# Optimization experiments

Measured on AMD Instinct MI355X. Metric: run time of the kernel, lower is better.

## Reference

```python
import jax, jax.numpy as jnp
import numpy as np

B, N, C, H = 4, 1024, 1024, 16
D = C // H  # head_dim = 64


def _xavier(key, shape, gain):
    fan_in, fan_out = shape[1], shape[0]
    limit = gain * np.sqrt(6.0 / (fan_in + fan_out))
    return jax.random.uniform(key, shape, jnp.float32, -limit, limit)


def setup_inputs() -> dict:
    key = jax.random.key(0)
    ks = jax.random.split(key, 12)
    g = 2.0 ** (-0.5)
    return {
        "x": jax.random.normal(ks[0], (B, N, C), jnp.float32),
        "attn_bias": jax.random.normal(ks[1], (B, H, N, N), jnp.float32),
        "attn_mask": jnp.ones((B, N), jnp.int32),
        "Wq": _xavier(ks[2], (C, C), g), "bq": jnp.zeros((C,), jnp.float32),
        "Wk": _xavier(ks[3], (C, C), g), "bk": jnp.zeros((C,), jnp.float32),
        "Wv": _xavier(ks[4], (C, C), g), "bv": jnp.zeros((C,), jnp.float32),
        "Wo": _xavier(ks[5], (C, C), 1.0), "bo": jnp.zeros((C,), jnp.float32),
    }


def reference(x, attn_bias, attn_mask, Wq, bq, Wk, bk, Wv, bv, Wo, bo):
    scale = D ** (-0.5)
    # projections; nn.Linear computes x @ W.T + b
    def proj(W, b):
        return (x @ W.T + b).reshape(B, N, H, D).transpose(0, 2, 1, 3)  # [B,H,N,D]
    q = proj(Wq, bq) * scale
    k = proj(Wk, bk)
    v = proj(Wv, bv)
    scores = jnp.einsum("bhnd,bhmd->bhnm", q, k)  # [B,H,N,N]
    scores = scores + attn_bias  # attn_bias_type == 'add'
    # 2D mask [B,N] -> [B,1,1,N]; masked_fill where mask == 0
    mask = attn_mask[:, None, None, :]
    scores = jnp.where(mask == 0, -jnp.inf, scores)
    weights = jax.nn.softmax(scores, axis=-1)  # stable (internal max subtract)
    # attn_drop is identity in eval / p=0.0
    out = jnp.einsum("bhnm,bhmd->bhnd", weights, v)
    out = out.transpose(0, 2, 1, 3).reshape(B, N, C)
    return out @ Wo.T + bo
```

## Files before the change

### kernel.cpp

```cpp
#include <hip/hip_runtime.h>
#include <hip/hip_bf16.h>

#define B_ 4
#define N_ 1024
#define C_ 1024
#define H_ 16
#define D_ 64

typedef __attribute__((ext_vector_type(8))) short bf16x8;
typedef __attribute__((ext_vector_type(4))) float f32x4;
typedef __attribute__((ext_vector_type(4))) int i32x4;

__device__ __forceinline__ void gld_lds16(const void* g, void* l) {
    __builtin_amdgcn_global_load_lds(
        (const __attribute__((address_space(1))) void*)g,
        (__attribute__((address_space(3))) void*)l, 16, 0, 0);
}

__device__ __forceinline__ unsigned cvt_pk_bf16(float lo, float hi) {
    unsigned r;
    asm("v_cvt_pk_bf16_f32 %0, %1, %2" : "=v"(r) : "v"(lo), "v"(hi));
    return r;
}

__global__ __launch_bounds__(256) void f2b_kernel(const float* __restrict__ s,
                                                  __hip_bfloat16* __restrict__ d,
                                                  int n) {
    int i = (blockIdx.x * 256 + threadIdx.x) * 4;
    if (i < n) {
        float4 v = *(const float4*)&s[i];
        d[i + 0] = __float2bfloat16(v.x);
        d[i + 1] = __float2bfloat16(v.y);
        d[i + 2] = __float2bfloat16(v.z);
        d[i + 3] = __float2bfloat16(v.w);
    }
}

__global__ __launch_bounds__(256) void f2b4_kernel(const float* __restrict__ w0,
                                                   const float* __restrict__ w1,
                                                   const float* __restrict__ w2,
                                                   const float* __restrict__ w3,
                                                   __hip_bfloat16* __restrict__ d0,
                                                   __hip_bfloat16* __restrict__ d1,
                                                   __hip_bfloat16* __restrict__ d2,
                                                   __hip_bfloat16* __restrict__ d3) {
    int sel = blockIdx.y;
    const float* s = sel == 0 ? w0 : sel == 1 ? w1 : sel == 2 ? w2 : w3;
    __hip_bfloat16* d = sel == 0 ? d0 : sel == 1 ? d1 : sel == 2 ? d2 : d3;
    int i = (blockIdx.x * 256 + threadIdx.x) * 4;
    float4 v = *(const float4*)&s[i];
    d[i + 0] = __float2bfloat16(v.x);
    d[i + 1] = __float2bfloat16(v.y);
    d[i + 2] = __float2bfloat16(v.z);
    d[i + 3] = __float2bfloat16(v.w);
}

__global__ __launch_bounds__(256) void gemm_qkv(const __hip_bfloat16* __restrict__ A,
                                                const __hip_bfloat16* __restrict__ wq,
                                                const __hip_bfloat16* __restrict__ wk,
                                                const __hip_bfloat16* __restrict__ wv,
                                                const float* __restrict__ bq,
                                                const float* __restrict__ bk,
                                                const float* __restrict__ bv,
                                                __hip_bfloat16* __restrict__ qo,
                                                __hip_bfloat16* __restrict__ ko,
                                                __hip_bfloat16* __restrict__ vto) {
    __shared__ __hip_bfloat16 Al[128 * 32];
    __shared__ __hip_bfloat16 Bl[128 * 32];
    const int sel = blockIdx.x >> 3;
    const __hip_bfloat16* Bw = sel == 0 ? wq : sel == 1 ? wk : wv;
    const float* bias = sel == 0 ? bq : sel == 1 ? bk : bv;
    const int t = threadIdx.x, w = t >> 6, l = t & 63;
    const int wr = w >> 1, wc = w & 1, lr = l & 15, lg = l >> 4;
    const int m0 = blockIdx.y * 128, n0 = (blockIdx.x & 7) * 128;
    const int K = C_;

    f32x4 acc[4][4] = {};

    for (int k0 = 0; k0 < K; k0 += 32) {
#pragma unroll
        for (int it = 0; it < 2; ++it) {
            int i = t + it * 256;
            int r = i >> 2, c8 = (i & 3) * 8;
            gld_lds16(A + (size_t)(m0 + r) * K + k0 + c8, &Al[i * 8]);
            gld_lds16(Bw + (size_t)(n0 + r) * K + k0 + c8, &Bl[i * 8]);
        }
        __syncthreads();
        bf16x8 af[4], bfr[4];
#pragma unroll
        for (int mi = 0; mi < 4; ++mi)
            af[mi] = *(const bf16x8*)&Al[(wr * 64 + mi * 16 + lr) * 32 + lg * 8];
#pragma unroll
        for (int ni = 0; ni < 4; ++ni)
            bfr[ni] = *(const bf16x8*)&Bl[(wc * 64 + ni * 16 + lr) * 32 + lg * 8];
#pragma unroll
        for (int mi = 0; mi < 4; ++mi)
#pragma unroll
            for (int ni = 0; ni < 4; ++ni)
                acc[mi][ni] = __builtin_amdgcn_mfma_f32_16x16x32_bf16(
                    af[mi], bfr[ni], acc[mi][ni], 0, 0, 0);
        __syncthreads();
    }

#pragma unroll
    for (int mi = 0; mi < 4; ++mi) {
#pragma unroll
        for (int ni = 0; ni < 4; ++ni) {
            int col = n0 + wc * 64 + ni * 16 + lr;
            float bb = bias[col];
#pragma unroll
            for (int j = 0; j < 4; ++j) {
                int row = m0 + wr * 64 + mi * 16 + lg * 4 + j;
                float v = acc[mi][ni][j] + bb;
                int bb_ = row >> 10, nn = row & 1023;
                int hh = col >> 6, dd = col & 63;
                if (sel == 0) {
                    qo[(((size_t)bb_ * H_ + hh) * N_ + nn) * D_ + dd] =
                        __float2bfloat16(v * 0.125f);
                } else if (sel == 1) {
                    ko[(((size_t)bb_ * H_ + hh) * N_ + nn) * D_ + dd] =
                        __float2bfloat16(v);
                } else {
                    vto[(((size_t)bb_ * H_ + hh) * D_ + dd) * N_ + nn] =
                        __float2bfloat16(v);
                }
            }
        }
    }
}

__global__ __launch_bounds__(256) void gemm_out(const __hip_bfloat16* __restrict__ A,
                                                const __hip_bfloat16* __restrict__ Bw,
                                                const float* __restrict__ bias,
                                                float* __restrict__ out) {
    __shared__ __hip_bfloat16 Al[128 * 32];
    __shared__ __hip_bfloat16 Bl[128 * 32];
    const int t = threadIdx.x, w = t >> 6, l = t & 63;
    const int wr = w >> 1, wc = w & 1, lr = l & 15, lg = l >> 4;
    const int m0 = blockIdx.y * 128, n0 = blockIdx.x * 128;
    const int K = C_;

    f32x4 acc[4][4] = {};

    for (int k0 = 0; k0 < K; k0 += 32) {
#pragma unroll
        for (int it = 0; it < 2; ++it) {
            int i = t + it * 256;
            int r = i >> 2, c8 = (i & 3) * 8;
            gld_lds16(A + (size_t)(m0 + r) * K + k0 + c8, &Al[i * 8]);
            gld_lds16(Bw + (size_t)(n0 + r) * K + k0 + c8, &Bl[i * 8]);
        }
        __syncthreads();
        bf16x8 af[4], bfr[4];
#pragma unroll
        for (int mi = 0; mi < 4; ++mi)
            af[mi] = *(const bf16x8*)&Al[(wr * 64 + mi * 16 + lr) * 32 + lg * 8];
#pragma unroll
        for (int ni = 0; ni < 4; ++ni)
            bfr[ni] = *(const bf16x8*)&Bl[(wc * 64 + ni * 16 + lr) * 32 + lg * 8];
#pragma unroll
        for (int mi = 0; mi < 4; ++mi)
#pragma unroll
            for (int ni = 0; ni < 4; ++ni)
                acc[mi][ni] = __builtin_amdgcn_mfma_f32_16x16x32_bf16(
                    af[mi], bfr[ni], acc[mi][ni], 0, 0, 0);
        __syncthreads();
    }

#pragma unroll
    for (int mi = 0; mi < 4; ++mi)
#pragma unroll
        for (int ni = 0; ni < 4; ++ni) {
            int col = n0 + wc * 64 + ni * 16 + lr;
            float bb = bias[col];
#pragma unroll
            for (int j = 0; j < 4; ++j) {
                int row = m0 + wr * 64 + mi * 16 + lg * 4 + j;
                out[(size_t)row * C_ + col] = acc[mi][ni][j] + bb;
            }
        }
}

#define ATTN_ITER(KT, CB, SB)                                                      \
    {                                                                              \
        const int ktn_ = (KT) < 15 ? (KT) + 1 : 15;                                \
        gld_lds16(kg0 + (size_t)ktn_ * 4096, &Kl[SB][(w * 64) * 8]);               \
        gld_lds16(vg0 + ktn_ * 64, &Vl[SB][(w * 64) * 8]);                         \
        __builtin_amdgcn_sched_barrier(0);                                         \
        asm volatile("s_waitcnt vmcnt(6)" ::: "memory");                           \
        __builtin_amdgcn_sched_barrier(0);                                         \
        __builtin_amdgcn_s_barrier();                                              \
        __builtin_amdgcn_sched_barrier(0);                                         \
        const __hip_bfloat16* Kb = &Kl[CB][0];                                     \
        f32x4 a_[4];                                                               \
        __builtin_amdgcn_s_setprio(1);                                             \
        _Pragma("unroll")                                                          \
        for (int nkb = 0; nkb < 4; ++nkb) {                                        \
            f32x4 a = {};                                                          \
            _Pragma("unroll")                                                      \
            for (int half = 0; half < 2; ++half) {                                 \
                bf16x8 kf = *(const bf16x8*)                                       \
                    &Kb[(nkb * 16 + lr) * 64 + ((half * 32 + lg * 8) ^ swz)];      \
                a = __builtin_amdgcn_mfma_f32_16x16x32_bf16(kf, qf[half], a,       \
                                                            0, 0, 0);              \
            }                                                                      \
            a_[nkb] = a;                                                           \
        }                                                                          \
        __builtin_amdgcn_s_setprio(0);                                             \
        __builtin_amdgcn_sched_barrier(0);                                         \
        asm volatile("s_waitcnt vmcnt(2)" ::: "memory");                           \
        __builtin_amdgcn_sched_barrier(0);                                         \
        float s[4][4];                                                             \
        _Pragma("unroll")                                                          \
        for (int nkb = 0; nkb < 4; ++nkb) {                                        \
            f32x4 bb = *(const f32x4*)&Bb[w][lr][((nkb * 4 + lg) ^ lr) * 4];       \
            f32x4 pen = *(const f32x4*)&Pen[(KT) * 64 + nkb * 16 + lg * 4];        \
            _Pragma("unroll")                                                      \
            for (int j = 0; j < 4; ++j) s[nkb][j] = a_[nkb][j] + bb[j] + pen[j];   \
        }                                                                          \
        __builtin_amdgcn_sched_barrier(0);                                         \
        asm volatile("s_waitcnt lgkmcnt(0)" ::: "memory");                         \
        __builtin_amdgcn_sched_barrier(0);                                         \
        _Pragma("unroll")                                                          \
        for (int i_ = 0; i_ < 4; ++i_)                                             \
            gld_lds16(bg[i_] + ktn_ * 64, bl + i_ * 256);                          \
        __builtin_amdgcn_sched_barrier(0);                                         \
        float tm = s[0][0];                                                        \
        _Pragma("unroll")                                                          \
        for (int nkb = 0; nkb < 4; ++nkb)                                          \
            _Pragma("unroll")                                                      \
            for (int j = 0; j < 4; ++j) tm = fmaxf(tm, s[nkb][j]);                 \
        tm = fmaxf(tm, __shfl_xor(tm, 16));                                        \
        tm = fmaxf(tm, __shfl_xor(tm, 32));                                        \
        const float mn = fmaxf(m_, tm);                                            \
        const float al = __expf(m_ - mn);                                          \
        m_ = mn;                                                                   \
        float ts = 0.f;                                                            \
        _Pragma("unroll")                                                          \
        for (int nkb = 0; nkb < 4; ++nkb)                                          \
            _Pragma("unroll")                                                      \
            for (int j = 0; j < 4; ++j) {                                          \
                float p = __expf(s[nkb][j] - mn);                                  \
                s[nkb][j] = p;                                                     \
                ts += p;                                                           \
            }                                                                      \
        ts += __shfl_xor(ts, 16);                                                  \
        ts += __shfl_xor(ts, 32);                                                  \
        l_ = l_ * al + ts;                                                         \
        unsigned pk0[4], pk1[4];                                                   \
        _Pragma("unroll")                                                          \
        for (int nkb = 0; nkb < 4; ++nkb) {                                        \
            pk0[nkb] = cvt_pk_bf16(s[nkb][0], s[nkb][1]);                          \
            pk1[nkb] = cvt_pk_bf16(s[nkb][2], s[nkb][3]);                          \
        }                                                                          \
        float alr[4];                                                              \
        _Pragma("unroll")                                                          \
        for (int j = 0; j < 4; ++j) alr[j] = __shfl(al, lg * 4 + j);               \
        _Pragma("unroll")                                                          \
        for (int db = 0; db < 4; ++db)                                             \
            _Pragma("unroll")                                                      \
            for (int j = 0; j < 4; ++j) acc[db][j] *= alr[j];                      \
        const __hip_bfloat16* Vb = &Vl[CB][0];                                     \
        __builtin_amdgcn_s_setprio(1);                                             \
        _Pragma("unroll")                                                          \
        for (int mh = 0; mh < 2; ++mh) {                                           \
            const int n0_ = 2 * mh, n1_ = 2 * mh + 1;                              \
            int e0a = __shfl((int)pk0[n0_], shi0), e0b = __shfl((int)pk0[n1_], shi0); \
            int e1a = __shfl((int)pk1[n0_], shi0), e1b = __shfl((int)pk1[n1_], shi0); \
            int e2a = __shfl((int)pk0[n0_], shi1), e2b = __shfl((int)pk0[n1_], shi1); \
            int e3a = __shfl((int)pk1[n0_], shi1), e3b = __shfl((int)pk1[n1_], shi1); \
            i32x4 pw;                                                              \
            pw[0] = lghi ? e0b : e0a;                                              \
            pw[1] = lghi ? e1b : e1a;                                              \
            pw[2] = lghi ? e2b : e2a;                                              \
            pw[3] = lghi ? e3b : e3a;                                              \
            bf16x8 paf = *(bf16x8*)&pw;                                            \
            _Pragma("unroll")                                                      \
            for (int db = 0; db < 4; ++db) {                                       \
                bf16x8 vf = *(const bf16x8*)                                       \
                    &Vb[(db * 16 + lr) * 64 + ((mh * 32 + lg * 8) ^ swz)];         \
                acc[db] = __builtin_amdgcn_mfma_f32_16x16x32_bf16(paf, vf,         \
                                                                  acc[db], 0, 0,  \
                                                                  0);              \
            }                                                                      \
        }                                                                          \
        __builtin_amdgcn_s_setprio(0);                                             \
        __builtin_amdgcn_sched_barrier(0);                                         \
        __builtin_amdgcn_s_barrier();                                              \
        __builtin_amdgcn_sched_barrier(0);                                         \
    }

__global__ __launch_bounds__(512, 4) void attn_kernel(const __hip_bfloat16* __restrict__ q,
                                                      const __hip_bfloat16* __restrict__ k,
                                                      const __hip_bfloat16* __restrict__ vt,
                                                      const float* __restrict__ bias,
                                                      const int* __restrict__ mask,
                                                      __hip_bfloat16* __restrict__ ao) {
    const int orig = blockIdx.x;
    const int wg = (orig & 7) * 64 + (orig >> 3);
    const int qt = wg & 7, h = (wg >> 3) & 15, b = wg >> 7;
    const int t = threadIdx.x, w = t >> 6, l = t & 63;
    const int lr = l & 15, lg = l >> 4;

    __shared__ __hip_bfloat16 Kl[2][64 * 64];
    __shared__ __hip_bfloat16 Vl[2][64 * 64];
    __shared__ float Pen[1024];
    __shared__ float Bb[8][16][64];

    const size_t bh = (size_t)b * H_ + h;
    const int qr0 = qt * 128;
    const int myrow = qr0 + w * 16 + lr;
    const int orow_base = qr0 + w * 16 + lg * 4;

    {
        int2 mi = *(const int2*)&mask[b * N_ + t * 2];
        float2 p;
        p.x = mi.x ? 0.f : -1e30f;
        p.y = mi.y ? 0.f : -1e30f;
        *(float2*)&Pen[t * 2] = p;
    }
    __syncthreads();

    const int r0 = t >> 3;
    const int e0 = ((t & 7) * 8) ^ ((r0 & 7) << 3);
    const __hip_bfloat16* kg0 = k + (bh * N_ + r0) * D_ + e0;
    const __hip_bfloat16* vg0 = vt + (bh * D_ + r0) * N_ + e0;

    const int rb = l >> 4, pb = l & 15;
    const float* bg[4];
#pragma unroll
    for (int i = 0; i < 4; ++i) {
        int ri = i * 4 + rb;
        bg[i] = bias + ((size_t)bh * N_ + qr0 + w * 16 + ri) * N_ + (pb ^ ri) * 4;
    }
    float* bl = &Bb[w][0][0];

    bf16x8 qf[2];
#pragma unroll
    for (int half = 0; half < 2; ++half)
        qf[half] = *(const bf16x8*)&q[(bh * N_ + myrow) * D_ + half * 32 + lg * 8];

    const int swz = (lr & 7) << 3;
    const int shi0 = ((lg & 1) << 5) + lr;
    const int shi1 = shi0 + 16;
    const bool lghi = (lg >> 1) != 0;

    f32x4 acc[4] = {};
    float m_ = -3e38f, l_ = 0.f;

    __builtin_amdgcn_sched_barrier(0);
    gld_lds16(kg0, &Kl[0][(w * 64) * 8]);
    gld_lds16(vg0, &Vl[0][(w * 64) * 8]);
#pragma unroll
    for (int i = 0; i < 4; ++i) gld_lds16(bg[i], bl + i * 256);
    __builtin_amdgcn_sched_barrier(0);

    for (int kt = 0; kt < 16; kt += 2) {
        ATTN_ITER(kt, 0, 1);
        ATTN_ITER(kt + 1, 1, 0);
    }

    float linv[4];
#pragma unroll
    for (int j = 0; j < 4; ++j) linv[j] = 1.f / __shfl(l_, lg * 4 + j);
#pragma unroll
    for (int db = 0; db < 4; ++db)
#pragma unroll
        for (int j = 0; j < 4; ++j)
            ao[((size_t)b * N_ + orow_base + j) * C_ + h * 64 + db * 16 + lr] =
                __float2bfloat16(acc[db][j] * linv[j]);
}

extern "C" void kernel_launch(void* const* d_in, const int* in_sizes, int n_in,
                              void* d_out, int out_size, void* d_ws, size_t ws_size,
                              hipStream_t stream) {
    const float* x    = (const float*)d_in[0];
    const float* bias = (const float*)d_in[1];
    const int*   mask = (const int*)d_in[2];
    const float* Wq   = (const float*)d_in[3];
    const float* bq   = (const float*)d_in[4];
    const float* Wk   = (const float*)d_in[5];
    const float* bk   = (const float*)d_in[6];
    const float* Wv   = (const float*)d_in[7];
    const float* bv   = (const float*)d_in[8];
    const float* Wo   = (const float*)d_in[9];
    const float* bo   = (const float*)d_in[10];
    float* out = (float*)d_out;

    char* ws = (char*)d_ws;
    const size_t MB = 1u << 20;
    __hip_bfloat16* xb  = (__hip_bfloat16*)(ws + 0 * MB);
    __hip_bfloat16* wqb = (__hip_bfloat16*)(ws + 8 * MB);
    __hip_bfloat16* wkb = (__hip_bfloat16*)(ws + 10 * MB);
    __hip_bfloat16* wvb = (__hip_bfloat16*)(ws + 12 * MB);
    __hip_bfloat16* wob = (__hip_bfloat16*)(ws + 14 * MB);
    __hip_bfloat16* qb  = (__hip_bfloat16*)(ws + 16 * MB);
    __hip_bfloat16* kb  = (__hip_bfloat16*)(ws + 24 * MB);
    __hip_bfloat16* vtb = (__hip_bfloat16*)(ws + 32 * MB);
    __hip_bfloat16* aob = (__hip_bfloat16*)(ws + 40 * MB);

    f2b_kernel<<<4096, 256, 0, stream>>>(x, xb, B_ * N_ * C_);
    f2b4_kernel<<<dim3(1024, 4), 256, 0, stream>>>(Wq, Wk, Wv, Wo, wqb, wkb, wvb, wob);

    gemm_qkv<<<dim3(24, 32), 256, 0, stream>>>(xb, wqb, wkb, wvb, bq, bk, bv, qb, kb, vtb);

    attn_kernel<<<512, 512, 0, stream>>>(qb, kb, vtb, bias, mask, aob);

    gemm_out<<<dim3(8, 32), 256, 0, stream>>>(aob, wob, bo, out);
}
```

Measured before the change: 154.0 us.

## Prefetch attention bias into registers and triple-buffer K/V to drop a barrier

Attention bias tiles now go straight from global memory into a two-deep register double buffer, loaded two tiles ahead, instead of being staged through a per-wave LDS buffer with extra waitcnts. K/V LDS buffers go from two to three, so the trailing workgroup barrier at the end of each tile iteration can be removed, and the loop is unrolled by six. This cuts LDS traffic and synchronisation for the bias. The cost is more vector registers, less coalesced per-row bias reads, and reliance on compiler-inserted vmcnt waits next to the hand-placed vmcnt(6).

```diff
diff --git a/kernel.cpp b/kernel.cpp
--- a/kernel.cpp
+++ b/kernel.cpp
@@ -181,9 +181,10 @@
         }
 }
 
-#define ATTN_ITER(KT, CB, SB)                                                      \
+#define ATTN_ITER(KT, CB, SB, BCUR)                                                \
     {                                                                              \
         const int ktn_ = (KT) < 15 ? (KT) + 1 : 15;                                \
+        const int ktb_ = (KT) < 14 ? (KT) + 2 : 15;                                \
         gld_lds16(kg0 + (size_t)ktn_ * 4096, &Kl[SB][(w * 64) * 8]);               \
         gld_lds16(vg0 + ktn_ * 64, &Vl[SB][(w * 64) * 8]);                         \
         __builtin_amdgcn_sched_barrier(0);                                         \
@@ -192,7 +193,7 @@
         __builtin_amdgcn_s_barrier();                                              \
         __builtin_amdgcn_sched_barrier(0);                                         \
         const __hip_bfloat16* Kb = &Kl[CB][0];                                     \
-        f32x4 a_[4];                                                               \
+        float s[4][4];                                                             \
         __builtin_amdgcn_s_setprio(1);                                             \
         _Pragma("unroll")                                                          \
         for (int nkb = 0; nkb < 4; ++nkb) {                                        \
@@ -204,26 +205,15 @@
                 a = __builtin_amdgcn_mfma_f32_16x16x32_bf16(kf, qf[half], a,       \
                                                             0, 0, 0);              \
             }                                                                      \
-            a_[nkb] = a;                                                           \
+            f32x4 pen = *(const f32x4*)&Pen[(KT) * 64 + nkb * 16 + lg * 4];        \
+            _Pragma("unroll")                                                      \
+            for (int j = 0; j < 4; ++j) s[nkb][j] = a[j] + BCUR[nkb][j] + pen[j];  \
         }                                                                          \
         __builtin_amdgcn_s_setprio(0);                                             \
         __builtin_amdgcn_sched_barrier(0);                                         \
-        asm volatile("s_waitcnt vmcnt(2)" ::: "memory");                           \
-        __builtin_amdgcn_sched_barrier(0);                                         \
-        float s[4][4];                                                             \
-        _Pragma("unroll")                                                          \
-        for (int nkb = 0; nkb < 4; ++nkb) {                                        \
-            f32x4 bb = *(const f32x4*)&Bb[w][lr][((nkb * 4 + lg) ^ lr) * 4];       \
-            f32x4 pen = *(const f32x4*)&Pen[(KT) * 64 + nkb * 16 + lg * 4];        \
-            _Pragma("unroll")                                                      \
-            for (int j = 0; j < 4; ++j) s[nkb][j] = a_[nkb][j] + bb[j] + pen[j];   \
-        }                                                                          \
-        __builtin_amdgcn_sched_barrier(0);                                         \
-        asm volatile("s_waitcnt lgkmcnt(0)" ::: "memory");                         \
-        __builtin_amdgcn_sched_barrier(0);                                         \
-        _Pragma("unroll")                                                          \
-        for (int i_ = 0; i_ < 4; ++i_)                                             \
-            gld_lds16(bg[i_] + ktn_ * 64, bl + i_ * 256);                          \
+        _Pragma("unroll")                                                          \
+        for (int nkb = 0; nkb < 4; ++nkb)                                          \
+            BCUR[nkb] = *(const f32x4*)&brow[ktb_ * 64 + nkb * 16 + lg * 4];       \
         __builtin_amdgcn_sched_barrier(0);                                         \
         float tm = s[0][0];                                                        \
         _Pragma("unroll")                                                          \
@@ -286,8 +276,6 @@
         }                                                                          \
         __builtin_amdgcn_s_setprio(0);                                             \
         __builtin_amdgcn_sched_barrier(0);                                         \
-        __builtin_amdgcn_s_barrier();                                              \
-        __builtin_amdgcn_sched_barrier(0);                                         \
     }
 
 __global__ __launch_bounds__(512, 4) void attn_kernel(const __hip_bfloat16* __restrict__ q,
@@ -302,10 +290,9 @@
     const int t = threadIdx.x, w = t >> 6, l = t & 63;
     const int lr = l & 15, lg = l >> 4;
 
-    __shared__ __hip_bfloat16 Kl[2][64 * 64];
-    __shared__ __hip_bfloat16 Vl[2][64 * 64];
+    __shared__ __hip_bfloat16 Kl[3][64 * 64];
+    __shared__ __hip_bfloat16 Vl[3][64 * 64];
     __shared__ float Pen[1024];
-    __shared__ float Bb[8][16][64];
 
     const size_t bh = (size_t)b * H_ + h;
     const int qr0 = qt * 128;
@@ -326,20 +313,12 @@
     const __hip_bfloat16* kg0 = k + (bh * N_ + r0) * D_ + e0;
     const __hip_bfloat16* vg0 = vt + (bh * D_ + r0) * N_ + e0;
 
-    const int rb = l >> 4, pb = l & 15;
-    const float* bg[4];
-#pragma unroll
-    for (int i = 0; i < 4; ++i) {
-        int ri = i * 4 + rb;
-        bg[i] = bias + ((size_t)bh * N_ + qr0 + w * 16 + ri) * N_ + (pb ^ ri) * 4;
-    }
-    float* bl = &Bb[w][0][0];
-
     bf16x8 qf[2];
 #pragma unroll
     for (int half = 0; half < 2; ++half)
         qf[half] = *(const bf16x8*)&q[(bh * N_ + myrow) * D_ + half * 32 + lg * 8];
 
+    const float* brow = bias + ((size_t)bh * N_ + myrow) * N_;
     const int swz = (lr & 7) << 3;
     const int shi0 = ((lg & 1) << 5) + lr;
     const int shi1 = shi0 + 16;
@@ -351,14 +330,30 @@
     __builtin_amdgcn_sched_barrier(0);
     gld_lds16(kg0, &Kl[0][(w * 64) * 8]);
     gld_lds16(vg0, &Vl[0][(w * 64) * 8]);
-#pragma unroll
-    for (int i = 0; i < 4; ++i) gld_lds16(bg[i], bl + i * 256);
+    f32x4 bA[4], bB[4];
+#pragma unroll
+    for (int nkb = 0; nkb < 4; ++nkb) {
+        bA[nkb] = *(const f32x4*)&brow[nkb * 16 + lg * 4];
+        bB[nkb] = *(const f32x4*)&brow[64 + nkb * 16 + lg * 4];
+    }
     __builtin_amdgcn_sched_barrier(0);
 
-    for (int kt = 0; kt < 16; kt += 2) {
-        ATTN_ITER(kt, 0, 1);
-        ATTN_ITER(kt + 1, 1, 0);
-    }
+    for (int kt = 0; kt < 12; kt += 6) {
+        ATTN_ITER(kt + 0, 0, 1, bA);
+        ATTN_ITER(kt + 1, 1, 2, bB);
+        ATTN_ITER(kt + 2, 2, 0, bA);
+        ATTN_ITER(kt + 3, 0, 1, bB);
+        ATTN_ITER(kt + 4, 1, 2, bA);
+        ATTN_ITER(kt + 5, 2, 0, bB);
+    }
+    ATTN_ITER(12, 0, 1, bA);
+    ATTN_ITER(13, 1, 2, bB);
+    ATTN_ITER(14, 2, 0, bA);
+    ATTN_ITER(15, 0, 1, bB);
+
+    float dummy = bA[0][0] + bA[1][0] + bA[2][0] + bA[3][0] +
+                  bB[0][0] + bB[1][0] + bB[2][0] + bB[3][0];
+    asm volatile("" :: "v"(dummy));
 
     float linv[4];
 #pragma unroll
```

Measured after the change: 165.3 us. +7.4%, slower.
